# Kernel optimization log

Hardware: AMD Instinct MI355X
Metric: run time of the kernel (lower is better)

## Reference

```python
import jax, jax.numpy as jnp
import numpy as np

B, C, H, W = 16, 256, 64, 64
NUM_HEADS = 4
GROUPS = 8
EPS = 1e-5


def setup_inputs() -> dict:
    key = jax.random.key(0)
    ks = jax.random.split(key, 7)
    x = jax.random.normal(ks[0], (B, C, H, W), dtype=jnp.float32)
    # GroupNorm affine params (torch default: weight=1, bias=0; randomize slightly for a stronger test)
    norm_w = jnp.ones((C,), jnp.float32) + 0.1 * jax.random.normal(ks[1], (C,), jnp.float32)
    norm_b = 0.1 * jax.random.normal(ks[2], (C,), jnp.float32)
    # 1x1 convs == channel GEMMs; kaiming-uniform-ish init scale
    s = 1.0 / np.sqrt(C)
    qkv_w = jax.random.uniform(ks[3], (3 * C, C), jnp.float32, -s, s)
    qkv_b = jax.random.uniform(ks[4], (3 * C,), jnp.float32, -s, s)
    proj_w = jax.random.uniform(ks[5], (C, C), jnp.float32, -s, s)
    proj_b = jax.random.uniform(ks[6], (C,), jnp.float32, -s, s)
    return {"x": x, "norm_w": norm_w, "norm_b": norm_b,
            "qkv_w": qkv_w, "qkv_b": qkv_b, "proj_w": proj_w, "proj_b": proj_b}


def reference(x, norm_w, norm_b, qkv_w, qkv_b, proj_w, proj_b):
    b, c, h, w = x.shape
    nh = NUM_HEADS
    dh = c // nh
    n = h * w
    # GroupNorm(8, C)
    xg = x.reshape(b, GROUPS, c // GROUPS, h, w)
    mean = xg.mean(axis=(2, 3, 4), keepdims=True)
    var = xg.var(axis=(2, 3, 4), keepdims=True)
    xn = ((xg - mean) * jax.lax.rsqrt(var + EPS)).reshape(b, c, h, w)
    xn = xn * norm_w[None, :, None, None] + norm_b[None, :, None, None]
    # QKV 1x1 conv as channel GEMM
    qkv = jnp.einsum('bchw,oc->bohw', xn, qkv_w) + qkv_b[None, :, None, None]
    qkv = qkv.reshape(b, 3, nh, dh, n)
    q, k, v = qkv[:, 0], qkv[:, 1], qkv[:, 2]  # each (B, nh, dh, N)
    scale = dh ** (-0.5)
    # Faithful to original einsum labeling: contracts over spatial axis,
    # attention matrix is over the HEADS axis: attn (B, dh, nh, nh)
    attn = jnp.einsum('bnhd,bmhd->bhnm', q * scale, k)
    attn = jax.nn.softmax(attn, axis=-1)
    out = jnp.einsum('bhnm,bmhd->bnhd', attn, v).reshape(b, c, h, w)
    return jnp.einsum('bchw,oc->bohw', out, proj_w) + proj_b[None, :, None, None] + x
```

## Files before the change

kernel.cpp:

```cpp
#include <hip/hip_runtime.h>
#include <stdint.h>

#define BB 16
#define CC 256
#define PP 4096

typedef __attribute__((ext_vector_type(4))) float f32x4;
typedef __attribute__((ext_vector_type(8))) short bf16x8;

static __device__ __forceinline__ float bf2f(unsigned short u) {
    union { uint32_t i; float f; } w; w.i = ((uint32_t)u) << 16; return w.f;
}
static __device__ __forceinline__ unsigned short f2bf(float f) {
    union { float f; uint32_t i; } w; w.f = f;
    uint32_t u = w.i;
    uint32_t r = u + 0x7FFFu + ((u >> 16) & 1u);
    return (unsigned short)(r >> 16);
}
static __device__ __forceinline__ float dot4(f32x4 a, f32x4 b) {
    return a.x * b.x + a.y * b.y + a.z * b.z + a.w * b.w;
}

__global__ void gn_partial_k(const float* __restrict__ x, float* __restrict__ Sx,
                             float* __restrict__ Sxx) {
    int ch0 = blockIdx.x * 8;
    int t = threadIdx.x;
    int lc = t >> 5, l32 = t & 31;
    int ch = ch0 + lc;
    const f32x4* v = (const f32x4*)(x + (size_t)ch * PP);
    float s = 0.f, ss = 0.f;
    for (int i = l32; i < PP / 4; i += 32) {
        f32x4 tv = v[i];
        s  += tv.x + tv.y + tv.z + tv.w;
        ss += tv.x * tv.x + tv.y * tv.y + tv.z * tv.z + tv.w * tv.w;
    }
    for (int off = 16; off > 0; off >>= 1) {
        s  += __shfl_down(s, off, 32);
        ss += __shfl_down(ss, off, 32);
    }
    if (l32 == 0) { Sx[ch] = s; Sxx[ch] = ss; }
}

__global__ void gn_final_k(const float* __restrict__ Sx, const float* __restrict__ Sxx,
                           const float* __restrict__ nw, const float* __restrict__ nb,
                           float* __restrict__ a_s, float* __restrict__ b_s,
                           float* __restrict__ s_vec) {
    int b = blockIdx.x, c = threadIdx.x;
    __shared__ float lsx[256], lsxx[256];
    float mySx = Sx[b * CC + c];
    lsx[c] = mySx; lsxx[c] = Sxx[b * CC + c];
    __syncthreads();
    int g0 = (c >> 5) << 5;
    float S = 0.f, SS = 0.f;
    for (int j = 0; j < 32; j++) { S += lsx[g0 + j]; SS += lsxx[g0 + j]; }
    const float inv = 1.0f / 131072.0f;
    float mean = S * inv;
    float var = SS * inv - mean * mean;
    float rstd = rsqrtf(var + 1e-5f);
    float w = nw[c];
    float a = rstd * w;
    float sh = nb[c] - mean * rstd * w;
    a_s[b * CC + c] = a;
    b_s[b * CC + c] = sh;
    s_vec[b * CC + c] = a * mySx + 4096.0f * sh;
}

__global__ void cvt_bf16_k(const float* __restrict__ in, unsigned short* __restrict__ out, int n) {
    int i = blockIdx.x * 256 + threadIdx.x;
    if (i < n) out[i] = f2bf(in[i]);
}

__global__ void wvt_k(const float* __restrict__ Wv, unsigned short* __restrict__ WvT) {
    int tc1 = blockIdx.x & 3, tc2 = blockIdx.x >> 2;
    int c1_0 = tc1 * 64, c2_0 = tc2 * 64;
    __shared__ unsigned short T[64][65];
    int t = threadIdx.x;
    int r = t >> 2, q = (t & 3) * 16;
    for (int j = 0; j < 4; j++) {
        f32x4 v = *(const f32x4*)(Wv + (size_t)(c1_0 + r) * 256 + c2_0 + q + j * 4);
        T[r][q + j * 4 + 0] = f2bf(v.x);
        T[r][q + j * 4 + 1] = f2bf(v.y);
        T[r][q + j * 4 + 2] = f2bf(v.z);
        T[r][q + j * 4 + 3] = f2bf(v.w);
    }
    __syncthreads();
    union { unsigned short h[16]; uint4 u[2]; } buf;
    for (int j = 0; j < 16; j++) buf.h[j] = T[q + j][r];
    unsigned short* dst = WvT + (size_t)(c2_0 + r) * 256 + c1_0 + q;
    *(uint4*)dst       = buf.u[0];
    *(uint4*)(dst + 8) = buf.u[1];
}

__global__ void xnt_k(const float* __restrict__ x, const float* __restrict__ a_s,
                      const float* __restrict__ b_s, unsigned short* __restrict__ xnT,
                      unsigned short* __restrict__ xnC) {
    int pt = blockIdx.x & 63, ct = (blockIdx.x >> 6) & 3, b = blockIdx.x >> 8;
    int c0 = ct * 64, p0 = pt * 64;
    __shared__ unsigned short T[64][66];
    int t = threadIdx.x;
    int cl = t >> 4, pl4 = (t & 15) * 4;
    for (int i = 0; i < 4; i++) {
        int c = c0 + i * 16 + cl;
        float a = a_s[b * CC + c], sh = b_s[b * CC + c];
        f32x4 v = *(const f32x4*)(x + ((size_t)b * CC + c) * PP + p0 + pl4);
        ushort4 u;
        u.x = f2bf(a * v.x + sh);
        u.y = f2bf(a * v.y + sh);
        u.z = f2bf(a * v.z + sh);
        u.w = f2bf(a * v.w + sh);
        T[i * 16 + cl][pl4 + 0] = u.x;
        T[i * 16 + cl][pl4 + 1] = u.y;
        T[i * 16 + cl][pl4 + 2] = u.z;
        T[i * 16 + cl][pl4 + 3] = u.w;
        *(ushort4*)(xnC + ((size_t)b * CC + c) * PP + p0 + pl4) = u;
    }
    __syncthreads();
    int pl = t >> 2, c16 = (t & 3) * 16;
    union { unsigned short h[16]; uint4 u[2]; } buf;
    for (int j = 0; j < 16; j++) buf.h[j] = T[c16 + j][pl];
    unsigned short* dst = xnT + ((size_t)b * PP + p0 + pl) * CC + c0 + c16;
    *(uint4*)dst       = buf.u[0];
    *(uint4*)(dst + 8) = buf.u[1];
}

static __device__ __forceinline__ void gemm_core(const unsigned short* __restrict__ Rg,
                                                 const unsigned short* __restrict__ Cg,
                                                 int kLen, int rstride,
                                                 f32x4 (&acc)[4][4]) {
    __shared__ unsigned short Rs[128][32];
    __shared__ unsigned short Cs[128][32];
    int t = threadIdx.x;
    int lane = t & 63, wave = t >> 6;
    int wm = wave >> 1, wn = wave & 1;
    int lr = lane & 15, lq = lane >> 4;
    int srow = t >> 2;
    int ssl = ((t & 3) ^ ((t >> 3) & 3)) * 8;
    int sd  = (t & 3) * 8;
    int fsw = (lr >> 1) & 3;
    for (int mi = 0; mi < 4; mi++)
        for (int ni = 0; ni < 4; ni++) {
            acc[mi][ni][0] = 0.f; acc[mi][ni][1] = 0.f;
            acc[mi][ni][2] = 0.f; acc[mi][ni][3] = 0.f;
        }
    const unsigned short* gr0 = Rg + (size_t)srow * rstride + ssl;
    const unsigned short* gr1 = gr0 + (size_t)64 * rstride;
    const unsigned short* gc0 = Cg + (size_t)srow * rstride + ssl;
    const unsigned short* gc1 = gc0 + (size_t)64 * rstride;
    uint4 ra0 = *(const uint4*)(gr0);
    uint4 ra1 = *(const uint4*)(gr1);
    uint4 rc0 = *(const uint4*)(gc0);
    uint4 rc1 = *(const uint4*)(gc1);
    for (int k0 = 0; k0 < kLen; k0 += 32) {
        __syncthreads();
        *(uint4*)&Rs[srow][sd]      = ra0;
        *(uint4*)&Rs[srow + 64][sd] = ra1;
        *(uint4*)&Cs[srow][sd]      = rc0;
        *(uint4*)&Cs[srow + 64][sd] = rc1;
        __syncthreads();
        int kn = k0 + 32;
        if (kn < kLen) {
            ra0 = *(const uint4*)(gr0 + kn);
            ra1 = *(const uint4*)(gr1 + kn);
            rc0 = *(const uint4*)(gc0 + kn);
            rc1 = *(const uint4*)(gc1 + kn);
        }
        bf16x8 af[4], bfr[4];
        for (int mi = 0; mi < 4; mi++)
            af[mi]  = *(const bf16x8*)&Rs[wm * 64 + mi * 16 + lr][(lq ^ fsw) * 8];
        for (int ni = 0; ni < 4; ni++)
            bfr[ni] = *(const bf16x8*)&Cs[wn * 64 + ni * 16 + lr][(lq ^ fsw) * 8];
        for (int mi = 0; mi < 4; mi++)
            for (int ni = 0; ni < 4; ni++)
                acc[mi][ni] = __builtin_amdgcn_mfma_f32_16x16x32_bf16(af[mi], bfr[ni], acc[mi][ni], 0, 0, 0);
    }
}

__global__ __launch_bounds__(256) void gram64_k(const unsigned short* __restrict__ xnC,
                                                unsigned short* __restrict__ Gb) {
    int tile = blockIdx.x & 15, b = blockIdx.x >> 4;
    int t1 = (tile & 3) * 64;
    int t2 = (tile >> 2) * 64;
    __shared__ unsigned short Rs[64][32];
    __shared__ unsigned short Cs[64][32];
    int t = threadIdx.x;
    int lane = t & 63, wave = t >> 6;
    int lr = lane & 15, lq = lane >> 4;
    int srow = t >> 2;
    int ssl = ((t & 3) ^ ((t >> 3) & 3)) * 8;
    int sd  = (t & 3) * 8;
    int fsw = (lr >> 1) & 3;
    f32x4 acc[4];
    for (int mi = 0; mi < 4; mi++) {
        acc[mi][0] = 0.f; acc[mi][1] = 0.f; acc[mi][2] = 0.f; acc[mi][3] = 0.f;
    }
    const unsigned short* grp = xnC + ((size_t)b * CC + t2 + srow) * PP + ssl;
    const unsigned short* gcp = xnC + ((size_t)b * CC + t1 + srow) * PP + ssl;
    uint4 ra = *(const uint4*)(grp);
    uint4 rc = *(const uint4*)(gcp);
    uint4 rb = *(const uint4*)(grp + 32);
    uint4 rd = *(const uint4*)(gcp + 32);
    for (int k0 = 0; k0 < PP; k0 += 32) {
        __syncthreads();
        *(uint4*)&Rs[srow][sd] = ra;
        *(uint4*)&Cs[srow][sd] = rc;
        ra = rb; rc = rd;
        int kn = k0 + 64;
        if (kn < PP) {
            rb = *(const uint4*)(grp + kn);
            rd = *(const uint4*)(gcp + kn);
        }
        __syncthreads();
        bf16x8 af[4];
        for (int mi = 0; mi < 4; mi++)
            af[mi] = *(const bf16x8*)&Rs[mi * 16 + lr][(lq ^ fsw) * 8];
        bf16x8 bfr = *(const bf16x8*)&Cs[wave * 16 + lr][(lq ^ fsw) * 8];
        for (int mi = 0; mi < 4; mi++)
            acc[mi] = __builtin_amdgcn_mfma_f32_16x16x32_bf16(af[mi], bfr, acc[mi], 0, 0, 0);
    }
    int c1 = t1 + wave * 16 + lr;
    for (int mi = 0; mi < 4; mi++) {
        int c2q = t2 + mi * 16 + lq * 4;
        ushort4 u;
        u.x = f2bf(acc[mi][0]);
        u.y = f2bf(acc[mi][1]);
        u.z = f2bf(acc[mi][2]);
        u.w = f2bf(acc[mi][3]);
        *(ushort4*)(Gb + ((size_t)b * 256 + c1) * 256 + c2q) = u;
    }
}

__global__ __launch_bounds__(256, 3) void u_gemm_k(const unsigned short* __restrict__ Gb,
                                                   const unsigned short* __restrict__ Wqkvb,
                                                   float* __restrict__ UT) {
    int t12 = blockIdx.x & 3, b = blockIdx.x >> 2;
    int t1 = (t12 >> 1) * 128;
    int t2 = (t12 & 1) * 128;
    f32x4 acc[4][4];
    gemm_core(Gb + ((size_t)b * 256 + t1) * 256,
              Wqkvb + (size_t)(256 + t2) * 256, 256, 256, acc);
    int t = threadIdx.x, lane = t & 63, wave = t >> 6;
    int wm = wave >> 1, wn = wave & 1, lr = lane & 15, lq = lane >> 4;
    for (int mi = 0; mi < 4; mi++) {
        int c1q = t1 + wm * 64 + mi * 16 + lq * 4;
        for (int ni = 0; ni < 4; ni++) {
            int kr = t2 + wn * 64 + ni * 16 + lr;
            *(f32x4*)(UT + ((size_t)b * 256 + kr) * 256 + c1q) = acc[mi][ni];
        }
    }
}

__global__ void scoresfin_k(const float* __restrict__ qkv_w, const float* __restrict__ qkv_b,
                            const float* __restrict__ UT, const float* __restrict__ s_vec,
                            float* __restrict__ attn) {
    int h = blockIdx.x & 63, b = blockIdx.x >> 6;
    int l = threadIdx.x;
    int c = l * 4;
    f32x4 sv = *(const f32x4*)(s_vec + b * CC + c);
    f32x4 wq[4], wk[4], ut[4];
    for (int n = 0; n < 4; n++) wq[n] = *(const f32x4*)(qkv_w + (size_t)(n * 64 + h) * 256 + c);
    for (int m = 0; m < 4; m++) wk[m] = *(const f32x4*)(qkv_w + (size_t)(256 + m * 64 + h) * 256 + c);
    for (int m = 0; m < 4; m++) ut[m] = *(const f32x4*)(UT + ((size_t)b * 256 + m * 64 + h) * 256 + c);
    float red[24];
    for (int n = 0; n < 4; n++)
        for (int m = 0; m < 4; m++) red[n * 4 + m] = dot4(wq[n], ut[m]);
    for (int n = 0; n < 4; n++) red[16 + n] = dot4(wq[n], sv);
    for (int m = 0; m < 4; m++) red[20 + m] = dot4(wk[m], sv);
    #pragma unroll
    for (int i = 0; i < 24; i++)
        for (int off = 32; off > 0; off >>= 1)
            red[i] += __shfl_xor(red[i], off);
    __shared__ float sred[24];
    if (l == 0)
        for (int i = 0; i < 24; i++) sred[i] = red[i];
    __syncthreads();
    if (l < 4) {
        int n = l;
        float bq = qkv_b[n * 64 + h];
        float dqn = sred[16 + n];
        float lg[4];
        for (int m = 0; m < 4; m++) {
            float bk = qkv_b[256 + m * 64 + h];
            lg[m] = 0.125f * (sred[n * 4 + m] + bq * sred[20 + m] + bk * dqn + 4096.0f * bq * bk);
        }
        float mx = fmaxf(fmaxf(lg[0], lg[1]), fmaxf(lg[2], lg[3]));
        float e0 = expf(lg[0] - mx), e1 = expf(lg[1] - mx);
        float e2 = expf(lg[2] - mx), e3 = expf(lg[3] - mx);
        float inv = 1.0f / (e0 + e1 + e2 + e3);
        float* dst = attn + ((size_t)(b * 64 + h) * 4 + n) * 4;
        dst[0] = e0 * inv; dst[1] = e1 * inv; dst[2] = e2 * inv; dst[3] = e3 * inv;
    }
}

__global__ void make_wp_k(const float* __restrict__ proj_w, const float* __restrict__ attn,
                          const float* __restrict__ qkv_b, const float* __restrict__ proj_b,
                          unsigned short* __restrict__ Wp, float* __restrict__ bias2) {
    int t = threadIdx.x;
    int o = blockIdx.x & 255, b = blockIdx.x >> 8;
    int m = t >> 6, hh = t & 63;
    float s = 0.f;
    for (int n = 0; n < 4; n++)
        s += proj_w[o * 256 + n * 64 + hh] * attn[((size_t)(b * 64 + hh) * 4 + n) * 4 + m];
    Wp[((size_t)b * 256 + o) * 256 + t] = f2bf(s);
    float contrib = s * qkv_b[512 + t];
    int lane = t & 63, wave = t >> 6;
    for (int off = 32; off > 0; off >>= 1) contrib += __shfl_down(contrib, off);
    __shared__ float red[4];
    if (lane == 0) red[wave] = contrib;
    __syncthreads();
    if (t == 0) bias2[b * 256 + o] = proj_b[o] + red[0] + red[1] + red[2] + red[3];
}

__global__ __launch_bounds__(256, 3) void make_wc_k(const unsigned short* __restrict__ WvT,
                                                    const unsigned short* __restrict__ Wp,
                                                    unsigned short* __restrict__ Wc) {
    int t12 = blockIdx.x & 3, b = blockIdx.x >> 2;
    int c20 = (t12 & 1) * 128;
    int o0  = (t12 >> 1) * 128;
    f32x4 acc[4][4];
    gemm_core(WvT + (size_t)c20 * 256, Wp + ((size_t)b * 256 + o0) * 256, 256, 256, acc);
    int t = threadIdx.x, lane = t & 63, wave = t >> 6;
    int wm = wave >> 1, wn = wave & 1, lr = lane & 15, lq = lane >> 4;
    for (int mi = 0; mi < 4; mi++) {
        int c2q = c20 + wm * 64 + mi * 16 + lq * 4;
        for (int ni = 0; ni < 4; ni++) {
            int o = o0 + wn * 64 + ni * 16 + lr;
            ushort4 u;
            u.x = f2bf(acc[mi][ni][0]);
            u.y = f2bf(acc[mi][ni][1]);
            u.z = f2bf(acc[mi][ni][2]);
            u.w = f2bf(acc[mi][ni][3]);
            *(ushort4*)(Wc + ((size_t)b * 256 + o) * 256 + c2q) = u;
        }
    }
}

__global__ __launch_bounds__(256, 3) void final_gemm_k(const unsigned short* __restrict__ Wc,
                                                       const unsigned short* __restrict__ xnT,
                                                       const float* __restrict__ bias2,
                                                       const float* __restrict__ x,
                                                       float* __restrict__ out) {
    int nt = blockIdx.x & 31;
    int rest = blockIdx.x >> 5;
    int mt = rest & 1;
    int b  = rest >> 1;
    int o0 = mt * 128, p0 = nt * 128;
    f32x4 acc[4][4];
    gemm_core(xnT + ((size_t)b * PP + p0) * 256, Wc + ((size_t)b * 256 + o0) * 256, 256, 256, acc);
    int t = threadIdx.x, lane = t & 63, wave = t >> 6;
    int wm = wave >> 1, wn = wave & 1, lr = lane & 15, lq = lane >> 4;
    for (int mi = 0; mi < 4; mi++) {
        int p4 = p0 + wm * 64 + mi * 16 + lq * 4;
        for (int ni = 0; ni < 4; ni++) {
            int o = o0 + wn * 64 + ni * 16 + lr;
            size_t idx = ((size_t)b * CC + o) * PP + p4;
            float bias = bias2[b * CC + o];
            f32x4 xv = *(const f32x4*)(x + idx);
            f32x4 r;
            r[0] = acc[mi][ni][0] + bias + xv[0];
            r[1] = acc[mi][ni][1] + bias + xv[1];
            r[2] = acc[mi][ni][2] + bias + xv[2];
            r[3] = acc[mi][ni][3] + bias + xv[3];
            *(f32x4*)(out + idx) = r;
        }
    }
}

extern "C" void kernel_launch(void* const* d_in, const int* in_sizes, int n_in,
                              void* d_out, int out_size, void* d_ws, size_t ws_size,
                              hipStream_t stream) {
    const float* x      = (const float*)d_in[0];
    const float* norm_w = (const float*)d_in[1];
    const float* norm_b = (const float*)d_in[2];
    const float* qkv_w  = (const float*)d_in[3];
    const float* qkv_b  = (const float*)d_in[4];
    const float* proj_w = (const float*)d_in[5];
    const float* proj_b = (const float*)d_in[6];
    float* out = (float*)d_out;

    char* ws = (char*)d_ws;
    size_t off = 0;
    auto alloc = [&](size_t bytes) {
        void* p = ws + off;
        off += (bytes + 255) & ~(size_t)255;
        return p;
    };
    float* Sx    = (float*)alloc(BB * CC * sizeof(float));
    float* Sxx   = (float*)alloc(BB * CC * sizeof(float));
    float* a_s   = (float*)alloc(BB * CC * sizeof(float));
    float* b_s   = (float*)alloc(BB * CC * sizeof(float));
    float* s_vec = (float*)alloc(BB * CC * sizeof(float));
    float* attn  = (float*)alloc((size_t)BB * 64 * 16 * sizeof(float));
    float* bias2 = (float*)alloc(BB * CC * sizeof(float));
    unsigned short* Wqkvb = (unsigned short*)alloc((size_t)768 * 256 * 2);
    unsigned short* WvT   = (unsigned short*)alloc((size_t)256 * 256 * 2);
    unsigned short* Wp    = (unsigned short*)alloc((size_t)BB * 65536 * 2);
    unsigned short* Wc    = (unsigned short*)alloc((size_t)BB * 65536 * 2);
    unsigned short* Gb    = (unsigned short*)alloc((size_t)BB * 65536 * 2);
    float*          UT    = (float*)alloc((size_t)BB * 65536 * 4);
    unsigned short* xnT   = (unsigned short*)alloc((size_t)BB * PP * CC * 2);
    unsigned short* xnC   = (unsigned short*)alloc((size_t)BB * PP * CC * 2);

    gn_partial_k<<<BB * CC / 8, 256, 0, stream>>>(x, Sx, Sxx);
    gn_final_k<<<BB, 256, 0, stream>>>(Sx, Sxx, norm_w, norm_b, a_s, b_s, s_vec);
    cvt_bf16_k<<<768, 256, 0, stream>>>(qkv_w, Wqkvb, 768 * 256);
    wvt_k<<<16, 256, 0, stream>>>(qkv_w + (size_t)512 * 256, WvT);
    xnt_k<<<4096, 256, 0, stream>>>(x, a_s, b_s, xnT, xnC);
    gram64_k<<<BB * 16, 256, 0, stream>>>(xnC, Gb);
    u_gemm_k<<<BB * 4, 256, 0, stream>>>(Gb, Wqkvb, UT);
    scoresfin_k<<<BB * 64, 64, 0, stream>>>(qkv_w, qkv_b, UT, s_vec, attn);
    make_wp_k<<<BB * 256, 256, 0, stream>>>(proj_w, attn, qkv_b, proj_b, Wp, bias2);
    make_wc_k<<<BB * 4, 256, 0, stream>>>(WvT, Wp, Wc);
    final_gemm_k<<<BB * 2 * 32, 256, 0, stream>>>(Wc, xnT, bias2, x, out);
}
```

Before: 250.6 us.

## Fold GroupNorm affine into Gram and weights, fuse stats with bf16 staging

GroupNorm statistics are now computed in the same pass that converts raw x to bf16 in both layouts, which removes the separate full read of x for statistics. The normalization is applied algebraically rather than to the activations: the per-channel scale and shift correct the raw Gram matrix (gcor_k), the per-channel scale is folded into the combined weight Wca, and the shift enters the bias through a new vector tv. The Gram GEMM is split four ways along the spatial dimension so more blocks run in parallel, at the cost of fp32 partial buffers and an extra reduction kernel. Using the raw-x Gram with mean corrections can lose precision when channel means are large.

```diff
diff --git a/kernel.cpp b/kernel.cpp
--- a/kernel.cpp
+++ b/kernel.cpp
@@ -8,9 +8,6 @@
 typedef __attribute__((ext_vector_type(4))) float f32x4;
 typedef __attribute__((ext_vector_type(8))) short bf16x8;
 
-static __device__ __forceinline__ float bf2f(unsigned short u) {
-    union { uint32_t i; float f; } w; w.i = ((uint32_t)u) << 16; return w.f;
-}
 static __device__ __forceinline__ unsigned short f2bf(float f) {
     union { float f; uint32_t i; } w; w.f = f;
     uint32_t u = w.i;
@@ -21,34 +18,60 @@
     return a.x * b.x + a.y * b.y + a.z * b.z + a.w * b.w;
 }
 
-__global__ void gn_partial_k(const float* __restrict__ x, float* __restrict__ Sx,
-                             float* __restrict__ Sxx) {
-    int ch0 = blockIdx.x * 8;
+__global__ void xstage_k(const float* __restrict__ x, unsigned short* __restrict__ xbT,
+                         unsigned short* __restrict__ xbC, float* __restrict__ Spart,
+                         float* __restrict__ SSpart) {
+    int pt = blockIdx.x & 63, ct = (blockIdx.x >> 6) & 3, b = blockIdx.x >> 8;
+    int c0 = ct * 64, p0 = pt * 64;
+    __shared__ unsigned short T[64][66];
     int t = threadIdx.x;
-    int lc = t >> 5, l32 = t & 31;
-    int ch = ch0 + lc;
-    const f32x4* v = (const f32x4*)(x + (size_t)ch * PP);
-    float s = 0.f, ss = 0.f;
-    for (int i = l32; i < PP / 4; i += 32) {
-        f32x4 tv = v[i];
-        s  += tv.x + tv.y + tv.z + tv.w;
-        ss += tv.x * tv.x + tv.y * tv.y + tv.z * tv.z + tv.w * tv.w;
-    }
-    for (int off = 16; off > 0; off >>= 1) {
-        s  += __shfl_down(s, off, 32);
-        ss += __shfl_down(ss, off, 32);
-    }
-    if (l32 == 0) { Sx[ch] = s; Sxx[ch] = ss; }
-}
-
-__global__ void gn_final_k(const float* __restrict__ Sx, const float* __restrict__ Sxx,
+    int cl = t >> 4, pl4 = (t & 15) * 4;
+    for (int i = 0; i < 4; i++) {
+        int c = c0 + i * 16 + cl;
+        f32x4 v = *(const f32x4*)(x + ((size_t)b * CC + c) * PP + p0 + pl4);
+        ushort4 u;
+        u.x = f2bf(v.x); u.y = f2bf(v.y); u.z = f2bf(v.z); u.w = f2bf(v.w);
+        T[i * 16 + cl][pl4 + 0] = u.x;
+        T[i * 16 + cl][pl4 + 1] = u.y;
+        T[i * 16 + cl][pl4 + 2] = u.z;
+        T[i * 16 + cl][pl4 + 3] = u.w;
+        *(ushort4*)(xbC + ((size_t)b * CC + c) * PP + p0 + pl4) = u;
+        float s  = v.x + v.y + v.z + v.w;
+        float ss = dot4(v, v);
+        for (int off = 8; off > 0; off >>= 1) {
+            s  += __shfl_down(s, off, 16);
+            ss += __shfl_down(ss, off, 16);
+        }
+        if ((t & 15) == 0) {
+            Spart [((size_t)(b * CC + c) << 6) + pt] = s;
+            SSpart[((size_t)(b * CC + c) << 6) + pt] = ss;
+        }
+    }
+    __syncthreads();
+    int pl = t >> 2, c16 = (t & 3) * 16;
+    union { unsigned short h[16]; uint4 u[2]; } buf;
+    for (int j = 0; j < 16; j++) buf.h[j] = T[c16 + j][pl];
+    unsigned short* dst = xbT + ((size_t)b * PP + p0 + pl) * CC + c0 + c16;
+    *(uint4*)dst       = buf.u[0];
+    *(uint4*)(dst + 8) = buf.u[1];
+}
+
+__global__ void gn_final_k(const float* __restrict__ Spart, const float* __restrict__ SSpart,
                            const float* __restrict__ nw, const float* __restrict__ nb,
                            float* __restrict__ a_s, float* __restrict__ b_s,
                            float* __restrict__ s_vec) {
     int b = blockIdx.x, c = threadIdx.x;
     __shared__ float lsx[256], lsxx[256];
-    float mySx = Sx[b * CC + c];
-    lsx[c] = mySx; lsxx[c] = Sxx[b * CC + c];
+    float mySx = 0.f, mySxx = 0.f;
+    const float* sp  = Spart  + ((size_t)(b * CC + c) << 6);
+    const float* ssp = SSpart + ((size_t)(b * CC + c) << 6);
+    for (int j = 0; j < 64; j += 4) {
+        f32x4 v = *(const f32x4*)(sp + j);
+        f32x4 w = *(const f32x4*)(ssp + j);
+        mySx  += v.x + v.y + v.z + v.w;
+        mySxx += w.x + w.y + w.z + w.w;
+    }
+    lsx[c] = mySx; lsxx[c] = mySxx;
     __syncthreads();
     int g0 = (c >> 5) << 5;
     float S = 0.f, SS = 0.f;
@@ -91,36 +114,19 @@
     *(uint4*)(dst + 8) = buf.u[1];
 }
 
-__global__ void xnt_k(const float* __restrict__ x, const float* __restrict__ a_s,
-                      const float* __restrict__ b_s, unsigned short* __restrict__ xnT,
-                      unsigned short* __restrict__ xnC) {
-    int pt = blockIdx.x & 63, ct = (blockIdx.x >> 6) & 3, b = blockIdx.x >> 8;
-    int c0 = ct * 64, p0 = pt * 64;
-    __shared__ unsigned short T[64][66];
-    int t = threadIdx.x;
-    int cl = t >> 4, pl4 = (t & 15) * 4;
-    for (int i = 0; i < 4; i++) {
-        int c = c0 + i * 16 + cl;
-        float a = a_s[b * CC + c], sh = b_s[b * CC + c];
-        f32x4 v = *(const f32x4*)(x + ((size_t)b * CC + c) * PP + p0 + pl4);
-        ushort4 u;
-        u.x = f2bf(a * v.x + sh);
-        u.y = f2bf(a * v.y + sh);
-        u.z = f2bf(a * v.z + sh);
-        u.w = f2bf(a * v.w + sh);
-        T[i * 16 + cl][pl4 + 0] = u.x;
-        T[i * 16 + cl][pl4 + 1] = u.y;
-        T[i * 16 + cl][pl4 + 2] = u.z;
-        T[i * 16 + cl][pl4 + 3] = u.w;
-        *(ushort4*)(xnC + ((size_t)b * CC + c) * PP + p0 + pl4) = u;
-    }
-    __syncthreads();
-    int pl = t >> 2, c16 = (t & 3) * 16;
-    union { unsigned short h[16]; uint4 u[2]; } buf;
-    for (int j = 0; j < 16; j++) buf.h[j] = T[c16 + j][pl];
-    unsigned short* dst = xnT + ((size_t)b * PP + p0 + pl) * CC + c0 + c16;
-    *(uint4*)dst       = buf.u[0];
-    *(uint4*)(dst + 8) = buf.u[1];
+__global__ void tvec_k(const float* __restrict__ Wv, const float* __restrict__ b_s,
+                       float* __restrict__ tv) {
+    int b = blockIdx.x, c1 = threadIdx.x;
+    __shared__ float shv[256];
+    shv[c1] = b_s[b * CC + c1];
+    __syncthreads();
+    const float* row = Wv + (size_t)c1 * 256;
+    float s = 0.f;
+    for (int j = 0; j < 256; j += 4) {
+        f32x4 v = *(const f32x4*)(row + j);
+        s += v.x * shv[j] + v.y * shv[j + 1] + v.z * shv[j + 2] + v.w * shv[j + 3];
+    }
+    tv[b * CC + c1] = s;
 }
 
 static __device__ __forceinline__ void gemm_core(const unsigned short* __restrict__ Rg,
@@ -175,9 +181,11 @@
     }
 }
 
-__global__ __launch_bounds__(256) void gram64_k(const unsigned short* __restrict__ xnC,
-                                                unsigned short* __restrict__ Gb) {
-    int tile = blockIdx.x & 15, b = blockIdx.x >> 4;
+__global__ __launch_bounds__(256) void gram2_k(const unsigned short* __restrict__ xbC,
+                                               float* __restrict__ Gxp) {
+    int tile = blockIdx.x & 15;
+    int kc   = (blockIdx.x >> 4) & 3;
+    int b    = blockIdx.x >> 6;
     int t1 = (tile & 3) * 64;
     int t2 = (tile >> 2) * 64;
     __shared__ unsigned short Rs[64][32];
@@ -193,19 +201,19 @@
     for (int mi = 0; mi < 4; mi++) {
         acc[mi][0] = 0.f; acc[mi][1] = 0.f; acc[mi][2] = 0.f; acc[mi][3] = 0.f;
     }
-    const unsigned short* grp = xnC + ((size_t)b * CC + t2 + srow) * PP + ssl;
-    const unsigned short* gcp = xnC + ((size_t)b * CC + t1 + srow) * PP + ssl;
+    const unsigned short* grp = xbC + ((size_t)b * CC + t2 + srow) * PP + kc * 1024 + ssl;
+    const unsigned short* gcp = xbC + ((size_t)b * CC + t1 + srow) * PP + kc * 1024 + ssl;
     uint4 ra = *(const uint4*)(grp);
     uint4 rc = *(const uint4*)(gcp);
     uint4 rb = *(const uint4*)(grp + 32);
     uint4 rd = *(const uint4*)(gcp + 32);
-    for (int k0 = 0; k0 < PP; k0 += 32) {
+    for (int k0 = 0; k0 < 1024; k0 += 32) {
         __syncthreads();
         *(uint4*)&Rs[srow][sd] = ra;
         *(uint4*)&Cs[srow][sd] = rc;
         ra = rb; rc = rd;
         int kn = k0 + 64;
-        if (kn < PP) {
+        if (kn < 1024) {
             rb = *(const uint4*)(grp + kn);
             rd = *(const uint4*)(gcp + kn);
         }
@@ -218,26 +226,46 @@
             acc[mi] = __builtin_amdgcn_mfma_f32_16x16x32_bf16(af[mi], bfr, acc[mi], 0, 0, 0);
     }
     int c1 = t1 + wave * 16 + lr;
+    float* dst = Gxp + ((size_t)(kc * 16 + b)) * 65536;
     for (int mi = 0; mi < 4; mi++) {
         int c2q = t2 + mi * 16 + lq * 4;
-        ushort4 u;
-        u.x = f2bf(acc[mi][0]);
-        u.y = f2bf(acc[mi][1]);
-        u.z = f2bf(acc[mi][2]);
-        u.w = f2bf(acc[mi][3]);
-        *(ushort4*)(Gb + ((size_t)b * 256 + c1) * 256 + c2q) = u;
-    }
+        *(f32x4*)(dst + (size_t)c1 * 256 + c2q) = acc[mi];
+    }
+}
+
+__global__ void gcor_k(const float* __restrict__ Gxp, const float* __restrict__ a_s,
+                       const float* __restrict__ b_s, const float* __restrict__ s_vec,
+                       unsigned short* __restrict__ Gb) {
+    int i4 = blockIdx.x * 256 + threadIdx.x;
+    int e  = i4 * 4;
+    int b  = e >> 16;
+    int c1 = (e >> 8) & 255;
+    int c2 = e & 255;
+    const size_t stride = (size_t)16 * 65536;
+    f32x4 g = *(const f32x4*)(Gxp + e);
+    g += *(const f32x4*)(Gxp + stride + e);
+    g += *(const f32x4*)(Gxp + 2 * stride + e);
+    g += *(const f32x4*)(Gxp + 3 * stride + e);
+    float a1  = a_s[b * CC + c1];
+    float sh1 = b_s[b * CC + c1];
+    float sv1 = s_vec[b * CC + c1];
+    f32x4 a2  = *(const f32x4*)(a_s + b * CC + c2);
+    f32x4 sh2 = *(const f32x4*)(b_s + b * CC + c2);
+    f32x4 sv2 = *(const f32x4*)(s_vec + b * CC + c2);
+    f32x4 r = a1 * g * a2 + sh1 * sv2 + sv1 * sh2 - 4096.0f * sh1 * sh2;
+    ushort4 u;
+    u.x = f2bf(r.x); u.y = f2bf(r.y); u.z = f2bf(r.z); u.w = f2bf(r.w);
+    *(ushort4*)(Gb + e) = u;
 }
 
 __global__ __launch_bounds__(256, 3) void u_gemm_k(const unsigned short* __restrict__ Gb,
-                                                   const unsigned short* __restrict__ Wqkvb,
+                                                   const unsigned short* __restrict__ Wkb,
                                                    float* __restrict__ UT) {
     int t12 = blockIdx.x & 3, b = blockIdx.x >> 2;
     int t1 = (t12 >> 1) * 128;
     int t2 = (t12 & 1) * 128;
     f32x4 acc[4][4];
-    gemm_core(Gb + ((size_t)b * 256 + t1) * 256,
-              Wqkvb + (size_t)(256 + t2) * 256, 256, 256, acc);
+    gemm_core(Gb + ((size_t)b * 256 + t1) * 256, Wkb + (size_t)t2 * 256, 256, 256, acc);
     int t = threadIdx.x, lane = t & 63, wave = t >> 6;
     int wm = wave >> 1, wn = wave & 1, lr = lane & 15, lq = lane >> 4;
     for (int mi = 0; mi < 4; mi++) {
@@ -293,7 +321,8 @@
 
 __global__ void make_wp_k(const float* __restrict__ proj_w, const float* __restrict__ attn,
                           const float* __restrict__ qkv_b, const float* __restrict__ proj_b,
-                          unsigned short* __restrict__ Wp, float* __restrict__ bias2) {
+                          const float* __restrict__ tv,
+                          unsigned short* __restrict__ Wp, float* __restrict__ bias3) {
     int t = threadIdx.x;
     int o = blockIdx.x & 255, b = blockIdx.x >> 8;
     int m = t >> 6, hh = t & 63;
@@ -301,18 +330,19 @@
     for (int n = 0; n < 4; n++)
         s += proj_w[o * 256 + n * 64 + hh] * attn[((size_t)(b * 64 + hh) * 4 + n) * 4 + m];
     Wp[((size_t)b * 256 + o) * 256 + t] = f2bf(s);
-    float contrib = s * qkv_b[512 + t];
+    float contrib = s * (qkv_b[512 + t] + tv[b * CC + t]);
     int lane = t & 63, wave = t >> 6;
     for (int off = 32; off > 0; off >>= 1) contrib += __shfl_down(contrib, off);
     __shared__ float red[4];
     if (lane == 0) red[wave] = contrib;
     __syncthreads();
-    if (t == 0) bias2[b * 256 + o] = proj_b[o] + red[0] + red[1] + red[2] + red[3];
+    if (t == 0) bias3[b * 256 + o] = proj_b[o] + red[0] + red[1] + red[2] + red[3];
 }
 
 __global__ __launch_bounds__(256, 3) void make_wc_k(const unsigned short* __restrict__ WvT,
                                                     const unsigned short* __restrict__ Wp,
-                                                    unsigned short* __restrict__ Wc) {
+                                                    const float* __restrict__ a_s,
+                                                    unsigned short* __restrict__ Wca) {
     int t12 = blockIdx.x & 3, b = blockIdx.x >> 2;
     int c20 = (t12 & 1) * 128;
     int o0  = (t12 >> 1) * 128;
@@ -322,21 +352,22 @@
     int wm = wave >> 1, wn = wave & 1, lr = lane & 15, lq = lane >> 4;
     for (int mi = 0; mi < 4; mi++) {
         int c2q = c20 + wm * 64 + mi * 16 + lq * 4;
+        f32x4 av = *(const f32x4*)(a_s + b * CC + c2q);
         for (int ni = 0; ni < 4; ni++) {
             int o = o0 + wn * 64 + ni * 16 + lr;
             ushort4 u;
-            u.x = f2bf(acc[mi][ni][0]);
-            u.y = f2bf(acc[mi][ni][1]);
-            u.z = f2bf(acc[mi][ni][2]);
-            u.w = f2bf(acc[mi][ni][3]);
-            *(ushort4*)(Wc + ((size_t)b * 256 + o) * 256 + c2q) = u;
-        }
-    }
-}
-
-__global__ __launch_bounds__(256, 3) void final_gemm_k(const unsigned short* __restrict__ Wc,
-                                                       const unsigned short* __restrict__ xnT,
-                                                       const float* __restrict__ bias2,
+            u.x = f2bf(acc[mi][ni][0] * av.x);
+            u.y = f2bf(acc[mi][ni][1] * av.y);
+            u.z = f2bf(acc[mi][ni][2] * av.z);
+            u.w = f2bf(acc[mi][ni][3] * av.w);
+            *(ushort4*)(Wca + ((size_t)b * 256 + o) * 256 + c2q) = u;
+        }
+    }
+}
+
+__global__ __launch_bounds__(256, 3) void final_gemm_k(const unsigned short* __restrict__ Wca,
+                                                       const unsigned short* __restrict__ xbT,
+                                                       const float* __restrict__ bias3,
                                                        const float* __restrict__ x,
                                                        float* __restrict__ out) {
     int nt = blockIdx.x & 31;
@@ -345,7 +376,7 @@
     int b  = rest >> 1;
     int o0 = mt * 128, p0 = nt * 128;
     f32x4 acc[4][4];
-    gemm_core(xnT + ((size_t)b * PP + p0) * 256, Wc + ((size_t)b * 256 + o0) * 256, 256, 256, acc);
+    gemm_core(xbT + ((size_t)b * PP + p0) * 256, Wca + ((size_t)b * 256 + o0) * 256, 256, 256, acc);
     int t = threadIdx.x, lane = t & 63, wave = t >> 6;
     int wm = wave >> 1, wn = wave & 1, lr = lane & 15, lq = lane >> 4;
     for (int mi = 0; mi < 4; mi++) {
@@ -353,7 +384,7 @@
         for (int ni = 0; ni < 4; ni++) {
             int o = o0 + wn * 64 + ni * 16 + lr;
             size_t idx = ((size_t)b * CC + o) * PP + p4;
-            float bias = bias2[b * CC + o];
+            float bias = bias3[b * CC + o];
             f32x4 xv = *(const f32x4*)(x + idx);
             f32x4 r;
             r[0] = acc[mi][ni][0] + bias + xv[0];
@@ -384,31 +415,34 @@
         off += (bytes + 255) & ~(size_t)255;
         return p;
     };
-    float* Sx    = (float*)alloc(BB * CC * sizeof(float));
-    float* Sxx   = (float*)alloc(BB * CC * sizeof(float));
-    float* a_s   = (float*)alloc(BB * CC * sizeof(float));
-    float* b_s   = (float*)alloc(BB * CC * sizeof(float));
-    float* s_vec = (float*)alloc(BB * CC * sizeof(float));
-    float* attn  = (float*)alloc((size_t)BB * 64 * 16 * sizeof(float));
-    float* bias2 = (float*)alloc(BB * CC * sizeof(float));
-    unsigned short* Wqkvb = (unsigned short*)alloc((size_t)768 * 256 * 2);
-    unsigned short* WvT   = (unsigned short*)alloc((size_t)256 * 256 * 2);
-    unsigned short* Wp    = (unsigned short*)alloc((size_t)BB * 65536 * 2);
-    unsigned short* Wc    = (unsigned short*)alloc((size_t)BB * 65536 * 2);
-    unsigned short* Gb    = (unsigned short*)alloc((size_t)BB * 65536 * 2);
-    float*          UT    = (float*)alloc((size_t)BB * 65536 * 4);
-    unsigned short* xnT   = (unsigned short*)alloc((size_t)BB * PP * CC * 2);
-    unsigned short* xnC   = (unsigned short*)alloc((size_t)BB * PP * CC * 2);
-
-    gn_partial_k<<<BB * CC / 8, 256, 0, stream>>>(x, Sx, Sxx);
-    gn_final_k<<<BB, 256, 0, stream>>>(Sx, Sxx, norm_w, norm_b, a_s, b_s, s_vec);
-    cvt_bf16_k<<<768, 256, 0, stream>>>(qkv_w, Wqkvb, 768 * 256);
+    float* Spart  = (float*)alloc((size_t)BB * CC * 64 * sizeof(float));
+    float* SSpart = (float*)alloc((size_t)BB * CC * 64 * sizeof(float));
+    float* a_s    = (float*)alloc(BB * CC * sizeof(float));
+    float* b_s    = (float*)alloc(BB * CC * sizeof(float));
+    float* s_vec  = (float*)alloc(BB * CC * sizeof(float));
+    float* tv     = (float*)alloc(BB * CC * sizeof(float));
+    float* attn   = (float*)alloc((size_t)BB * 64 * 16 * sizeof(float));
+    float* bias3  = (float*)alloc(BB * CC * sizeof(float));
+    unsigned short* Wkb = (unsigned short*)alloc((size_t)256 * 256 * 2);
+    unsigned short* WvT = (unsigned short*)alloc((size_t)256 * 256 * 2);
+    unsigned short* Wp  = (unsigned short*)alloc((size_t)BB * 65536 * 2);
+    unsigned short* Wca = (unsigned short*)alloc((size_t)BB * 65536 * 2);
+    unsigned short* Gb  = (unsigned short*)alloc((size_t)BB * 65536 * 2);
+    float*          UT  = (float*)alloc((size_t)BB * 65536 * 4);
+    float*          Gxp = (float*)alloc((size_t)4 * BB * 65536 * 4);
+    unsigned short* xbT = (unsigned short*)alloc((size_t)BB * PP * CC * 2);
+    unsigned short* xbC = (unsigned short*)alloc((size_t)BB * PP * CC * 2);
+
+    xstage_k<<<4096, 256, 0, stream>>>(x, xbT, xbC, Spart, SSpart);
+    gn_final_k<<<BB, 256, 0, stream>>>(Spart, SSpart, norm_w, norm_b, a_s, b_s, s_vec);
+    cvt_bf16_k<<<256, 256, 0, stream>>>(qkv_w + (size_t)256 * 256, Wkb, 256 * 256);
     wvt_k<<<16, 256, 0, stream>>>(qkv_w + (size_t)512 * 256, WvT);
-    xnt_k<<<4096, 256, 0, stream>>>(x, a_s, b_s, xnT, xnC);
-    gram64_k<<<BB * 16, 256, 0, stream>>>(xnC, Gb);
-    u_gemm_k<<<BB * 4, 256, 0, stream>>>(Gb, Wqkvb, UT);
+    tvec_k<<<BB, 256, 0, stream>>>(qkv_w + (size_t)512 * 256, b_s, tv);
+    gram2_k<<<BB * 16 * 4, 256, 0, stream>>>(xbC, Gxp);
+    gcor_k<<<1024, 256, 0, stream>>>(Gxp, a_s, b_s, s_vec, Gb);
+    u_gemm_k<<<BB * 4, 256, 0, stream>>>(Gb, Wkb, UT);
     scoresfin_k<<<BB * 64, 64, 0, stream>>>(qkv_w, qkv_b, UT, s_vec, attn);
-    make_wp_k<<<BB * 256, 256, 0, stream>>>(proj_w, attn, qkv_b, proj_b, Wp, bias2);
-    make_wc_k<<<BB * 4, 256, 0, stream>>>(WvT, Wp, Wc);
-    final_gemm_k<<<BB * 2 * 32, 256, 0, stream>>>(Wc, xnT, bias2, x, out);
-}
+    make_wp_k<<<BB * 256, 256, 0, stream>>>(proj_w, attn, qkv_b, proj_b, tv, Wp, bias3);
+    make_wc_k<<<BB * 4, 256, 0, stream>>>(WvT, Wp, a_s, Wca);
+    final_gemm_k<<<BB * 2 * 32, 256, 0, stream>>>(Wca, xbT, bias3, x, out);
+}
```

Measured after the change: 252.5 us. About the same (+0.8%).
